# Kernel tuning notes

Hardware: AMD Instinct MI355X
Metric: run time of the kernel (lower is better)

## Reference

```python
import jax, jax.numpy as jnp
import numpy as np

M = 0.25
GAMMA = 256.0
HARD_W = 2.0
O_P = 1.0 + M
O_N = -M
DELTA_P = 1.0 - M
DELTA_N = M
NEG_BIG = -1e30  # masked-out fill for logsumexp (finite to keep grads NaN-free)


def setup_inputs() -> dict:
    key = jax.random.key(0)
    k1, k2 = jax.random.split(key)
    inputs = jax.random.normal(k1, (4096, 512), dtype=jnp.float32)
    targets = jax.random.randint(k2, (4096,), 0, 64, dtype=jnp.int64)
    return {"inputs": inputs, "targets": targets}


def reference(inputs, targets):
    n = inputs.shape[0]
    x = inputs / jnp.linalg.norm(inputs, axis=1, keepdims=True)  # L2 normalize
    sim = x @ x.T                                                # [n, n]

    same = targets[:, None] == targets[None, :]
    eye = jnp.eye(n, dtype=bool)
    pos_mask = same & ~eye
    neg_mask = ~same
    npos = pos_mask.sum(axis=1)
    nneg = neg_mask.sum(axis=1)

    sim_d = jax.lax.stop_gradient(sim)  # alphas are detached in the original
    alpha_p = jax.nn.relu(O_P - sim_d)
    alpha_n = jax.nn.relu(sim_d - O_N)

    # hard mining: scale alpha at hardest positive (min sim) / hardest negative (max sim)
    idx = jnp.arange(n)
    hard_p = jnp.argmin(jnp.where(pos_mask, sim_d, jnp.inf), axis=1)
    hard_n = jnp.argmax(jnp.where(neg_mask, sim_d, -jnp.inf), axis=1)
    hit_p = (idx[None, :] == hard_p[:, None]) & (npos > 1)[:, None]
    hit_n = (idx[None, :] == hard_n[:, None]) & (nneg > 1)[:, None]
    alpha_p = alpha_p * jnp.where(hit_p, HARD_W, 1.0)
    alpha_n = alpha_n * jnp.where(hit_n, HARD_W, 1.0)

    pos_term = jnp.where(pos_mask, -GAMMA * alpha_p * (sim - DELTA_P), NEG_BIG)
    neg_term = jnp.where(neg_mask, GAMMA * alpha_n * (sim - DELTA_N), NEG_BIG)
    lse_p = jax.nn.logsumexp(pos_term, axis=1)
    lse_n = jax.nn.logsumexp(neg_term, axis=1)

    valid = (npos > 0) & (nneg > 0)
    per_row = jnp.where(valid, jax.nn.softplus(lse_p + lse_n), 0.0)
    n_valid = jnp.maximum(valid.sum(), 1)
    return per_row.sum() / n_valid.astype(per_row.dtype)
```

## Files before the change

kernel.cpp:

```cpp
#include <hip/hip_runtime.h>


#define GAMMA_ 256.0f
#define MASKT_  (-1.0e4f)
#define MINITP_ (-1.0e4f)
#define MASKP_  (-3.0e4f)

constexpr int N_ = 4096;
constexpr int D_ = 512;
constexpr int AST_ = 520;
constexpr int CCH_ = 16;

typedef __bf16 bf16x8 __attribute__((ext_vector_type(8)));
typedef float  f32x4  __attribute__((ext_vector_type(4)));
typedef const unsigned int __attribute__((address_space(1)))* gp_t;
typedef unsigned int       __attribute__((address_space(3)))* lp_t;

__device__ __forceinline__ float pos_q(float s) {
    float d = s - 1.0f;
    return fmaf(d * d, 256.0f, -16.0f);
}
__device__ __forceinline__ float neg_q(float s) {
    float q = fmaf(s * s, 256.0f, -16.0f);
    return (s >= -0.25f) ? q : 0.0f;
}
__device__ __forceinline__ void lse_merge(float m2, float S2, float& m, float& S) {
    float mm = fmaxf(m, m2);
    S = S * __expf(m - mm) + S2 * __expf(m2 - mm);
    m = mm;
}
__device__ __forceinline__ unsigned short f2bf(float f) {
    unsigned int u = __float_as_uint(f);
    unsigned int r = u + 0x7FFFu + ((u >> 16) & 1u);
    return (unsigned short)(r >> 16);
}

__global__ __launch_bounds__(256) void k_norm(const float* __restrict__ in,
                                              unsigned short* __restrict__ xb,
                                              float* __restrict__ acc) {
    const int row  = blockIdx.x * 4 + (threadIdx.x >> 6);
    const int lane = threadIdx.x & 63;
    const float4* src = (const float4*)(in + (size_t)row * D_) + lane * 2;
    float4 a = src[0], b = src[1];
    float ss = a.x*a.x + a.y*a.y + a.z*a.z + a.w*a.w
             + b.x*b.x + b.y*b.y + b.z*b.z + b.w*b.w;
    #pragma unroll
    for (int d = 32; d >= 1; d >>= 1) ss += __shfl_xor(ss, d);
    float rn = 1.0f / sqrtf(ss);
    float v[8] = {a.x, a.y, a.z, a.w, b.x, b.y, b.z, b.w};
    union { uint4 u; unsigned short us[8]; } pk;
    #pragma unroll
    for (int k = 0; k < 8; ++k) pk.us[k] = f2bf(v[k] * rn);
    *((uint4*)(xb + (size_t)row * D_) + lane) = pk.u;
    if (blockIdx.x == 0 && threadIdx.x < 4) acc[threadIdx.x] = 0.0f;
}

__global__ __launch_bounds__(256, 4) void k_mainG(const unsigned short* __restrict__ xb,
                                                  const int* __restrict__ tg,
                                                  float* __restrict__ part) {
    constexpr int NST = 16;
    __shared__ __align__(16) unsigned short Bs[2][16][AST_];

    const int tid  = threadIdx.x;
    const int wave = tid >> 6, lane = tid & 63;
    const int n16  = lane & 15, quad = lane >> 4;
    const int rg   = (int)blockIdx.x >> 4;
    const int cc   = (int)blockIdx.x & 15;
    const int rowBase = rg * 64 + wave * 16;
    const int colBase = cc * 256;

    bf16x8 af[16];
    {
        const bf16x8* ap = (const bf16x8*)(xb + (size_t)(rowBase + n16) * D_ + quad * 8);
        #pragma unroll
        for (int kk = 0; kk < 16; ++kk) af[kk] = ap[kk * 4];
    }
    int tr[4];
    #pragma unroll
    for (int r = 0; r < 4; ++r) tr[r] = tg[rowBase + quad * 4 + r];

    float m_p[4], S_p[4], m_n[4], S_n[4], mxn[4];
    #pragma unroll
    for (int r = 0; r < 4; ++r) {
        m_p[r] = MINITP_; S_p[r] = 0.f; m_n[r] = 0.f; S_n[r] = 0.f; mxn[r] = -2.0f;
    }

    const char* gstage = (const char*)xb + (size_t)colBase * 1024 + lane * 16;

    #pragma unroll
    for (int p = 0; p < 4; ++p) {
        int j = p * 4 + wave;
        __builtin_amdgcn_global_load_lds((gp_t)(const void*)(gstage + j * 1024),
                                         (lp_t)(void*)&Bs[0][j][0], 16, 0, 0);
    }
    int tc_cur = tg[colBase + n16];

    auto epi = [&](const f32x4& a0, const f32x4& a1, int tcv, bool withDiag) {
        #pragma unroll
        for (int r = 0; r < 4; ++r) {
            float sim = a0[r] + a1[r];
            bool samec = (tr[r] == tcv);
            float u = samec ? (sim - 1.0f) : sim;
            float t = fmaf(u * u, 256.0f, -16.0f);
            if (!samec && sim < -0.25f) t = 0.0f;
            if (withDiag && n16 == quad * 4 + r) t = MASKP_;
            float ms = samec ? m_p[r] : m_n[r];
            if (t > ms) {
                float scl = __expf(ms - t);
                if (samec) { S_p[r] = fmaf(S_p[r], scl, 1.0f); m_p[r] = t; }
                else       { S_n[r] = fmaf(S_n[r], scl, 1.0f); m_n[r] = t; }
            } else {
                float e = __expf(t - ms);
                S_p[r] += samec ? e : 0.0f;
                S_n[r] += samec ? 0.0f : e;
            }
            mxn[r] = fmaxf(mxn[r], samec ? -2.0f : sim);
        }
    };

    #pragma unroll 1
    for (int s = 0; s < NST; ++s) {
        const int b = s & 1;
        const int j0 = colBase + s * 16;
        __syncthreads();

        if (s + 1 < NST) {
            const char* g2 = gstage + (size_t)(s + 1) * 16 * 1024;
            #pragma unroll
            for (int p = 0; p < 4; ++p) {
                int j = p * 4 + wave;
                __builtin_amdgcn_global_load_lds((gp_t)(const void*)(g2 + j * 1024),
                                                 (lp_t)(void*)&Bs[b ^ 1][j][0], 16, 0, 0);
            }
        }
        int tc_nxt = (s + 1 < NST) ? tg[colBase + (s + 1) * 16 + n16] : 0;

        f32x4 a0 = {0.f, 0.f, 0.f, 0.f}, a1 = {0.f, 0.f, 0.f, 0.f};
        #pragma unroll
        for (int kk = 0; kk < 8; ++kk) {
            bf16x8 bf0 = *(const bf16x8*)&Bs[b][n16][(2 * kk) * 32 + quad * 8];
            bf16x8 bf1 = *(const bf16x8*)&Bs[b][n16][(2 * kk + 1) * 32 + quad * 8];
            a0 = __builtin_amdgcn_mfma_f32_16x16x32_bf16(af[2 * kk],     bf0, a0, 0, 0, 0);
            a1 = __builtin_amdgcn_mfma_f32_16x16x32_bf16(af[2 * kk + 1], bf1, a1, 0, 0, 0);
        }

        if (j0 == rowBase) epi(a0, a1, tc_cur, true);
        else               epi(a0, a1, tc_cur, false);
        tc_cur = tc_nxt;
    }

    #pragma unroll
    for (int r = 0; r < 4; ++r) {
        #pragma unroll
        for (int d = 1; d <= 8; d <<= 1) {
            lse_merge(__shfl_xor(m_p[r], d), __shfl_xor(S_p[r], d), m_p[r], S_p[r]);
            lse_merge(__shfl_xor(m_n[r], d), __shfl_xor(S_n[r], d), m_n[r], S_n[r]);
            mxn[r] = fmaxf(mxn[r], __shfl_xor(mxn[r], d));
        }
    }
    if (n16 == 0) {
        #pragma unroll
        for (int r = 0; r < 4; ++r) {
            ((float4*)part)[(size_t)(rowBase + quad * 4 + r) * CCH_ + cc] =
                make_float4(m_p[r], S_p[r], mxn[r], S_n[r]);
        }
    }
}

__global__ __launch_bounds__(256) void k_reduceF(const float* __restrict__ part,
                                                 const int* __restrict__ tg,
                                                 float* __restrict__ acc,
                                                 float* __restrict__ out) {
    __shared__ int hist[64];
    const int tid = threadIdx.x;
    if (tid < 64) hist[tid] = 0;
    __syncthreads();
    for (int i = tid; i < N_; i += 256) atomicAdd(&hist[tg[i]], 1);
    __syncthreads();

    const int row = blockIdx.x * 256 + tid;
    const float4* P = (const float4*)part + (size_t)row * CCH_;
    float M_p = MINITP_, Sp = 0.f, M_n = 0.f, Sn = 0.f, mxn = -2.0f;
    #pragma unroll
    for (int c = 0; c < CCH_; ++c) {
        float4 a = P[c];
        lse_merge(a.x, a.y, M_p, Sp);
        float mn = (a.z > -1.5f) ? fmaxf(neg_q(a.z), 0.0f) : 0.0f;
        lse_merge(mn, a.w, M_n, Sn);
        mxn = fmaxf(mxn, a.z);
    }
    const int cnt = hist[tg[row]];
    float np2 = (float)(cnt - 1), nn2 = (float)(N_ - cnt);
    float loss = 0.f, vld = 0.f;
    if (np2 > 0.5f && nn2 > 0.5f) {
        if (np2 > 1.5f) {
            float t1 = M_p, t2 = 2.0f * t1;
            float mm = fmaxf(M_p, t2);
            Sp = Sp * __expf(M_p - mm) + __expf(t2 - mm) - __expf(t1 - mm);
            M_p = mm;
        }
        if (nn2 > 1.5f) {
            float t1 = neg_q(mxn), t2 = 2.0f * t1;
            float mm = fmaxf(M_n, t2);
            Sn = Sn * __expf(M_n - mm) + __expf(t2 - mm) - __expf(t1 - mm);
            M_n = mm;
        }
        float z = (M_p + __logf(Sp)) + (M_n + __logf(Sn));
        loss = fmaxf(z, 0.0f) + log1pf(__expf(-fabsf(z)));
        vld = 1.0f;
    }
    #pragma unroll
    for (int d = 32; d >= 1; d >>= 1) { loss += __shfl_xor(loss, d); vld += __shfl_xor(vld, d); }
    if ((tid & 63) == 0) { atomicAdd(&acc[0], loss); atomicAdd(&acc[1], vld); }

    __syncthreads();
    if (tid == 0) {
        __threadfence();
        int old = atomicAdd((int*)(acc + 2), 1);
        if (old == (int)gridDim.x - 1) {
            float ls = atomicAdd(&acc[0], 0.0f);
            float lv = atomicAdd(&acc[1], 0.0f);
            out[0] = ls / fmaxf(lv, 1.0f);
        }
    }
}

__global__ void k_final(const float* __restrict__ acc, float* __restrict__ out) {
    if (threadIdx.x == 0) out[0] = acc[0] / fmaxf(acc[1], 1.0f);
}

__global__ void k_sentinel(float* __restrict__ out) {
    if (threadIdx.x == 0) out[0] = -12345.0f;
}

__global__ __launch_bounds__(1024, 4) void k_main3(const unsigned short* __restrict__ xb,
                                                   const int* __restrict__ tg,
                                                   float* __restrict__ acc_g) {
    __shared__ __align__(16) unsigned short As[16 * AST_];
    __shared__ float sm[16][16][8];
    const int tid  = threadIdx.x;
    const int wave = tid >> 6, lane = tid & 63;
    const int n16  = lane & 15, quad = lane >> 4;
    const int rowBase = blockIdx.x * 16;
    {
        int row = tid >> 6, c = tid & 63;
        *(uint4*)&As[row * AST_ + c * 8] =
            *(const uint4*)(xb + (size_t)(rowBase + row) * D_ + c * 8);
    }
    int ir[4], tr[4];
    #pragma unroll
    for (int r = 0; r < 4; ++r) { ir[r] = rowBase + quad * 4 + r; tr[r] = tg[ir[r]]; }
    float m_p[4], S_p[4], m_n[4], S_n[4], mnp[4], mxn[4], sc[4];
    #pragma unroll
    for (int r = 0; r < 4; ++r) {
        m_p[r] = 0.f; S_p[r] = 0.f; m_n[r] = 0.f; S_n[r] = 0.f;
        mnp[r] = 2.0f; mxn[r] = -2.0f; sc[r] = 0.f;
    }
    __syncthreads();
    const unsigned short* Af = &As[n16 * AST_ + quad * 8];
    #pragma unroll 1
    for (int t = wave; t < N_ / 16; t += 16) {
        const int jcol = t * 16 + n16;
        const int tc = tg[jcol];
        const bf16x8* bp = (const bf16x8*)(xb + (size_t)jcol * D_ + quad * 8);
        bf16x8 bf[16];
        #pragma unroll
        for (int kk = 0; kk < 16; ++kk) bf[kk] = bp[kk * 4];
        f32x4 a0 = {0.f, 0.f, 0.f, 0.f}, a1 = {0.f, 0.f, 0.f, 0.f};
        #pragma unroll
        for (int kk = 0; kk < 8; ++kk) {
            bf16x8 af0 = *(const bf16x8*)(Af + (2 * kk) * 32);
            bf16x8 af1 = *(const bf16x8*)(Af + (2 * kk + 1) * 32);
            a0 = __builtin_amdgcn_mfma_f32_16x16x32_bf16(af0, bf[2 * kk],     a0, 0, 0, 0);
            a1 = __builtin_amdgcn_mfma_f32_16x16x32_bf16(af1, bf[2 * kk + 1], a1, 0, 0, 0);
        }
        #pragma unroll
        for (int r = 0; r < 4; ++r) {
            float s = a0[r] + a1[r];
            bool samec = (tr[r] == tc);
            bool posm  = samec && (jcol != ir[r]);
            float tp = posm  ? pos_q(s) : MASKT_;
            float tn = samec ? MASKT_ : neg_q(s);
            float mm = fmaxf(m_p[r], tp);
            S_p[r] = S_p[r] * __expf(m_p[r] - mm) + __expf(tp - mm); m_p[r] = mm;
            mm = fmaxf(m_n[r], tn);
            S_n[r] = S_n[r] * __expf(m_n[r] - mm) + __expf(tn - mm); m_n[r] = mm;
            sc[r] += samec ? 1.0f : 0.0f;
            mnp[r] = fminf(mnp[r], posm ? s : 2.0f);
            mxn[r] = fmaxf(mxn[r], samec ? -2.0f : s);
        }
    }
    #pragma unroll
    for (int r = 0; r < 4; ++r) {
        #pragma unroll
        for (int d = 1; d <= 8; d <<= 1) {
            lse_merge(__shfl_xor(m_p[r], d), __shfl_xor(S_p[r], d), m_p[r], S_p[r]);
            lse_merge(__shfl_xor(m_n[r], d), __shfl_xor(S_n[r], d), m_n[r], S_n[r]);
            mnp[r] = fminf(mnp[r], __shfl_xor(mnp[r], d));
            mxn[r] = fmaxf(mxn[r], __shfl_xor(mxn[r], d));
            sc[r] += __shfl_xor(sc[r], d);
        }
    }
    if (n16 == 0) {
        #pragma unroll
        for (int r = 0; r < 4; ++r) {
            float* q = sm[wave][quad * 4 + r];
            q[0] = m_p[r]; q[1] = S_p[r]; q[2] = m_n[r]; q[3] = S_n[r];
            q[4] = mnp[r]; q[5] = mxn[r]; q[6] = sc[r];
        }
    }
    __syncthreads();
    if (tid < 64) {
        const int L = tid & 15;
        float m_p2 = 0.f, S_p2 = 0.f, m_n2 = 0.f, S_n2 = 0.f;
        float mnp2 = 2.0f, mxn2 = -2.0f, sct = 0.f;
        #pragma unroll
        for (int w = 0; w < 16; ++w) {
            const float* q = sm[w][L];
            lse_merge(q[0], q[1], m_p2, S_p2);
            lse_merge(q[2], q[3], m_n2, S_n2);
            mnp2 = fminf(mnp2, q[4]); mxn2 = fmaxf(mxn2, q[5]);
            sct += q[6];
        }
        float loss = 0.f, vld = 0.f;
        float np2 = sct - 1.0f, nn2 = (float)N_ - sct;
        if (tid < 16 && np2 > 0.5f && nn2 > 0.5f) {
            if (np2 > 1.5f) {
                float t1 = pos_q(mnp2), t2 = 2.0f * t1;
                float mm = fmaxf(m_p2, t2);
                S_p2 = S_p2 * __expf(m_p2 - mm) + __expf(t2 - mm) - __expf(t1 - mm);
                m_p2 = mm;
            }
            if (nn2 > 1.5f) {
                float t1 = neg_q(mxn2), t2 = 2.0f * t1;
                float mm = fmaxf(m_n2, t2);
                S_n2 = S_n2 * __expf(m_n2 - mm) + __expf(t2 - mm) - __expf(t1 - mm);
                m_n2 = mm;
            }
            float z = (m_p2 + __logf(S_p2)) + (m_n2 + __logf(S_n2));
            loss = fmaxf(z, 0.0f) + log1pf(__expf(-fabsf(z)));
            vld = 1.0f;
        }
        #pragma unroll
        for (int d = 32; d >= 1; d >>= 1) {
            loss += __shfl_xor(loss, d); vld += __shfl_xor(vld, d);
        }
        if (tid == 0) { atomicAdd(&acc_g[0], loss); atomicAdd(&acc_g[1], vld); }
    }
}

extern "C" void kernel_launch(void* const* d_in, const int* in_sizes, int n_in,
                              void* d_out, int out_size, void* d_ws, size_t ws_size,
                              hipStream_t stream) {
    const float* in = (const float*)d_in[0];
    const int*   tg = (const int*)d_in[1];
    constexpr size_t MB = 1024 * 1024;
    unsigned short* xb = (unsigned short*)d_ws;

    if (ws_size >= 5 * MB + 64) {
        float* part = (float*)((char*)d_ws + 4 * MB);
        float* acc  = (float*)((char*)d_ws + 5 * MB);
        hipLaunchKernelGGL(k_norm,    dim3(N_ / 4),    dim3(256), 0, stream, in, xb, acc);
        hipLaunchKernelGGL(k_mainG,   dim3(64 * CCH_), dim3(256), 0, stream, xb, tg, part);
        hipLaunchKernelGGL(k_reduceF, dim3(N_ / 256),  dim3(256), 0, stream, part, tg, acc,
                           (float*)d_out);
    } else if (ws_size >= 4 * MB + 64) {
        float* acc = (float*)((char*)d_ws + 4 * MB);
        hipLaunchKernelGGL(k_norm,  dim3(N_ / 4),  dim3(256),  0, stream, in, xb, acc);
        hipLaunchKernelGGL(k_main3, dim3(N_ / 16), dim3(1024), 0, stream, xb, tg, acc);
        hipLaunchKernelGGL(k_final, dim3(1),       dim3(64),   0, stream, acc, (float*)d_out);
    } else {
        hipLaunchKernelGGL(k_sentinel, dim3(1), dim3(64), 0, stream, (float*)d_out);
    }
}
```

Before: 106.9 us.

## Compute 32 rows per wave to reuse each LDS B tile twice

Each wave now holds two 16-row A fragment sets and runs four MFMA chains per 16-column step against the same LDS B tile. This halves the grid size and the number of times each column tile is staged and read per row. The cost is doubled A-fragment and accumulator register state, with launch bounds lowered to 2 blocks per CU. That reduces occupancy and the latency hiding available for the exp-heavy epilogue.

```diff
diff --git a/kernel.cpp b/kernel.cpp
--- a/kernel.cpp
+++ b/kernel.cpp
@@ -55,7 +55,7 @@
     if (blockIdx.x == 0 && threadIdx.x < 4) acc[threadIdx.x] = 0.0f;
 }
 
-__global__ __launch_bounds__(256, 4) void k_mainG(const unsigned short* __restrict__ xb,
+__global__ __launch_bounds__(256, 2) void k_mainH(const unsigned short* __restrict__ xb,
                                                   const int* __restrict__ tg,
                                                   float* __restrict__ part) {
     constexpr int NST = 16;
@@ -66,23 +66,26 @@
     const int n16  = lane & 15, quad = lane >> 4;
     const int rg   = (int)blockIdx.x >> 4;
     const int cc   = (int)blockIdx.x & 15;
-    const int rowBase = rg * 64 + wave * 16;
+    const int rowBase = rg * 128 + wave * 32;
     const int colBase = cc * 256;
 
-    bf16x8 af[16];
+    bf16x8 af0[16], af1[16];
     {
-        const bf16x8* ap = (const bf16x8*)(xb + (size_t)(rowBase + n16) * D_ + quad * 8);
-        #pragma unroll
-        for (int kk = 0; kk < 16; ++kk) af[kk] = ap[kk * 4];
-    }
-    int tr[4];
-    #pragma unroll
-    for (int r = 0; r < 4; ++r) tr[r] = tg[rowBase + quad * 4 + r];
-
-    float m_p[4], S_p[4], m_n[4], S_n[4], mxn[4];
-    #pragma unroll
-    for (int r = 0; r < 4; ++r) {
-        m_p[r] = MINITP_; S_p[r] = 0.f; m_n[r] = 0.f; S_n[r] = 0.f; mxn[r] = -2.0f;
+        const bf16x8* ap0 = (const bf16x8*)(xb + (size_t)(rowBase + n16) * D_ + quad * 8);
+        const bf16x8* ap1 = (const bf16x8*)(xb + (size_t)(rowBase + 16 + n16) * D_ + quad * 8);
+        #pragma unroll
+        for (int kk = 0; kk < 16; ++kk) { af0[kk] = ap0[kk * 4]; af1[kk] = ap1[kk * 4]; }
+    }
+    int tr[8];
+    #pragma unroll
+    for (int g = 0; g < 2; ++g)
+        #pragma unroll
+        for (int r = 0; r < 4; ++r) tr[g * 4 + r] = tg[rowBase + g * 16 + quad * 4 + r];
+
+    float m_p[8], S_p[8], m_n[8], S_n[8], mxn[8];
+    #pragma unroll
+    for (int i = 0; i < 8; ++i) {
+        m_p[i] = MINITP_; S_p[i] = 0.f; m_n[i] = 0.f; S_n[i] = 0.f; mxn[i] = -2.0f;
     }
 
     const char* gstage = (const char*)xb + (size_t)colBase * 1024 + lane * 16;
@@ -95,26 +98,26 @@
     }
     int tc_cur = tg[colBase + n16];
 
-    auto epi = [&](const f32x4& a0, const f32x4& a1, int tcv, bool withDiag) {
+    auto epi = [&](const f32x4& a0, const f32x4& a1, int tcv, bool withDiag, int base) {
         #pragma unroll
         for (int r = 0; r < 4; ++r) {
             float sim = a0[r] + a1[r];
-            bool samec = (tr[r] == tcv);
+            bool samec = (tr[base + r] == tcv);
             float u = samec ? (sim - 1.0f) : sim;
             float t = fmaf(u * u, 256.0f, -16.0f);
             if (!samec && sim < -0.25f) t = 0.0f;
             if (withDiag && n16 == quad * 4 + r) t = MASKP_;
-            float ms = samec ? m_p[r] : m_n[r];
+            float ms = samec ? m_p[base + r] : m_n[base + r];
             if (t > ms) {
                 float scl = __expf(ms - t);
-                if (samec) { S_p[r] = fmaf(S_p[r], scl, 1.0f); m_p[r] = t; }
-                else       { S_n[r] = fmaf(S_n[r], scl, 1.0f); m_n[r] = t; }
+                if (samec) { S_p[base + r] = fmaf(S_p[base + r], scl, 1.0f); m_p[base + r] = t; }
+                else       { S_n[base + r] = fmaf(S_n[base + r], scl, 1.0f); m_n[base + r] = t; }
             } else {
                 float e = __expf(t - ms);
-                S_p[r] += samec ? e : 0.0f;
-                S_n[r] += samec ? 0.0f : e;
-            }
-            mxn[r] = fmaxf(mxn[r], samec ? -2.0f : sim);
+                S_p[base + r] += samec ? e : 0.0f;
+                S_n[base + r] += samec ? 0.0f : e;
+            }
+            mxn[base + r] = fmaxf(mxn[base + r], samec ? -2.0f : sim);
         }
     };
 
@@ -136,34 +139,42 @@
         int tc_nxt = (s + 1 < NST) ? tg[colBase + (s + 1) * 16 + n16] : 0;
 
         f32x4 a0 = {0.f, 0.f, 0.f, 0.f}, a1 = {0.f, 0.f, 0.f, 0.f};
+        f32x4 a2 = {0.f, 0.f, 0.f, 0.f}, a3 = {0.f, 0.f, 0.f, 0.f};
         #pragma unroll
         for (int kk = 0; kk < 8; ++kk) {
             bf16x8 bf0 = *(const bf16x8*)&Bs[b][n16][(2 * kk) * 32 + quad * 8];
             bf16x8 bf1 = *(const bf16x8*)&Bs[b][n16][(2 * kk + 1) * 32 + quad * 8];
-            a0 = __builtin_amdgcn_mfma_f32_16x16x32_bf16(af[2 * kk],     bf0, a0, 0, 0, 0);
-            a1 = __builtin_amdgcn_mfma_f32_16x16x32_bf16(af[2 * kk + 1], bf1, a1, 0, 0, 0);
-        }
-
-        if (j0 == rowBase) epi(a0, a1, tc_cur, true);
-        else               epi(a0, a1, tc_cur, false);
+            a0 = __builtin_amdgcn_mfma_f32_16x16x32_bf16(af0[2 * kk],     bf0, a0, 0, 0, 0);
+            a1 = __builtin_amdgcn_mfma_f32_16x16x32_bf16(af0[2 * kk + 1], bf1, a1, 0, 0, 0);
+            a2 = __builtin_amdgcn_mfma_f32_16x16x32_bf16(af1[2 * kk],     bf0, a2, 0, 0, 0);
+            a3 = __builtin_amdgcn_mfma_f32_16x16x32_bf16(af1[2 * kk + 1], bf1, a3, 0, 0, 0);
+        }
+
+        if (j0 == rowBase)      epi(a0, a1, tc_cur, true,  0);
+        else                    epi(a0, a1, tc_cur, false, 0);
+        if (j0 == rowBase + 16) epi(a2, a3, tc_cur, true,  4);
+        else                    epi(a2, a3, tc_cur, false, 4);
         tc_cur = tc_nxt;
     }
 
     #pragma unroll
-    for (int r = 0; r < 4; ++r) {
+    for (int i = 0; i < 8; ++i) {
         #pragma unroll
         for (int d = 1; d <= 8; d <<= 1) {
-            lse_merge(__shfl_xor(m_p[r], d), __shfl_xor(S_p[r], d), m_p[r], S_p[r]);
-            lse_merge(__shfl_xor(m_n[r], d), __shfl_xor(S_n[r], d), m_n[r], S_n[r]);
-            mxn[r] = fmaxf(mxn[r], __shfl_xor(mxn[r], d));
+            lse_merge(__shfl_xor(m_p[i], d), __shfl_xor(S_p[i], d), m_p[i], S_p[i]);
+            lse_merge(__shfl_xor(m_n[i], d), __shfl_xor(S_n[i], d), m_n[i], S_n[i]);
+            mxn[i] = fmaxf(mxn[i], __shfl_xor(mxn[i], d));
         }
     }
     if (n16 == 0) {
         #pragma unroll
-        for (int r = 0; r < 4; ++r) {
-            ((float4*)part)[(size_t)(rowBase + quad * 4 + r) * CCH_ + cc] =
-                make_float4(m_p[r], S_p[r], mxn[r], S_n[r]);
-        }
+        for (int g = 0; g < 2; ++g)
+            #pragma unroll
+            for (int r = 0; r < 4; ++r) {
+                int i = g * 4 + r;
+                ((float4*)part)[(size_t)(rowBase + g * 16 + quad * 4 + r) * CCH_ + cc] =
+                    make_float4(m_p[i], S_p[i], mxn[i], S_n[i]);
+            }
     }
 }
 
@@ -361,7 +372,7 @@
         float* part = (float*)((char*)d_ws + 4 * MB);
         float* acc  = (float*)((char*)d_ws + 5 * MB);
         hipLaunchKernelGGL(k_norm,    dim3(N_ / 4),    dim3(256), 0, stream, in, xb, acc);
-        hipLaunchKernelGGL(k_mainG,   dim3(64 * CCH_), dim3(256), 0, stream, xb, tg, part);
+        hipLaunchKernelGGL(k_mainH,   dim3(32 * CCH_), dim3(256), 0, stream, xb, tg, part);
         hipLaunchKernelGGL(k_reduceF, dim3(N_ / 256),  dim3(256), 0, stream, part, tg, acc,
                            (float*)d_out);
     } else if (ws_size >= 4 * MB + 64) {
```

After: 110.2 us. 1.03x slower.

## Use base-2 exponent domain, stagger column tile order, raise MFMA priority

Applied to the files above, without the earlier changes.

Rescales the quadratic logit constants by 1/ln2 so every exponential becomes a native exp2 instead of __expf, which saves a multiply per exp in the hot epilogue. The log-sum-exp state now lives in the base-2 domain throughout, and the final value is converted back to natural log. It also rotates each block's starting column tile by a phase taken from the block index, spreading concurrent blocks across different B tiles to reduce L2/channel contention. It also sets s_setprio around the MFMA loop. These add complexity, and the constant rescaling carries a small rounding risk.

```diff
diff --git a/kernel.cpp b/kernel.cpp
--- a/kernel.cpp
+++ b/kernel.cpp
@@ -1,10 +1,12 @@
 #include <hip/hip_runtime.h>
 
 
-#define GAMMA_ 256.0f
 #define MASKT_  (-1.0e4f)
 #define MINITP_ (-1.0e4f)
 #define MASKP_  (-3.0e4f)
+#define QA_     369.3299304675f
+#define QB_     (-23.08312065422f)
+#define LN2_    0.6931471805599453f
 
 constexpr int N_ = 4096;
 constexpr int D_ = 512;
@@ -24,9 +26,18 @@
     float q = fmaf(s * s, 256.0f, -16.0f);
     return (s >= -0.25f) ? q : 0.0f;
 }
+__device__ __forceinline__ float neg_q2(float s) {
+    float q = fmaf(s * s, QA_, QB_);
+    return (s >= -0.25f) ? q : 0.0f;
+}
 __device__ __forceinline__ void lse_merge(float m2, float S2, float& m, float& S) {
     float mm = fmaxf(m, m2);
     S = S * __expf(m - mm) + S2 * __expf(m2 - mm);
+    m = mm;
+}
+__device__ __forceinline__ void lse_merge2(float m2, float S2, float& m, float& S) {
+    float mm = fmaxf(m, m2);
+    S = S * exp2f(m - mm) + S2 * exp2f(m2 - mm);
     m = mm;
 }
 __device__ __forceinline__ unsigned short f2bf(float f) {
@@ -55,7 +66,7 @@
     if (blockIdx.x == 0 && threadIdx.x < 4) acc[threadIdx.x] = 0.0f;
 }
 
-__global__ __launch_bounds__(256, 4) void k_mainG(const unsigned short* __restrict__ xb,
+__global__ __launch_bounds__(256, 4) void k_mainJ(const unsigned short* __restrict__ xb,
                                                   const int* __restrict__ tg,
                                                   float* __restrict__ part) {
     constexpr int NST = 16;
@@ -68,6 +79,7 @@
     const int cc   = (int)blockIdx.x & 15;
     const int rowBase = rg * 64 + wave * 16;
     const int colBase = cc * 256;
+    const int phase = (((int)blockIdx.x >> 8) & 3) * 4;
 
     bf16x8 af[16];
     {
@@ -87,13 +99,16 @@
 
     const char* gstage = (const char*)xb + (size_t)colBase * 1024 + lane * 16;
 
-    #pragma unroll
-    for (int p = 0; p < 4; ++p) {
-        int j = p * 4 + wave;
-        __builtin_amdgcn_global_load_lds((gp_t)(const void*)(gstage + j * 1024),
-                                         (lp_t)(void*)&Bs[0][j][0], 16, 0, 0);
-    }
-    int tc_cur = tg[colBase + n16];
+    {
+        const char* g0 = gstage + (size_t)phase * 16384;
+        #pragma unroll
+        for (int p = 0; p < 4; ++p) {
+            int j = p * 4 + wave;
+            __builtin_amdgcn_global_load_lds((gp_t)(const void*)(g0 + j * 1024),
+                                             (lp_t)(void*)&Bs[0][j][0], 16, 0, 0);
+        }
+    }
+    int tc_cur = tg[colBase + phase * 16 + n16];
 
     auto epi = [&](const f32x4& a0, const f32x4& a1, int tcv, bool withDiag) {
         #pragma unroll
@@ -101,16 +116,16 @@
             float sim = a0[r] + a1[r];
             bool samec = (tr[r] == tcv);
             float u = samec ? (sim - 1.0f) : sim;
-            float t = fmaf(u * u, 256.0f, -16.0f);
+            float t = fmaf(u * u, QA_, QB_);
             if (!samec && sim < -0.25f) t = 0.0f;
             if (withDiag && n16 == quad * 4 + r) t = MASKP_;
             float ms = samec ? m_p[r] : m_n[r];
             if (t > ms) {
-                float scl = __expf(ms - t);
+                float scl = exp2f(ms - t);
                 if (samec) { S_p[r] = fmaf(S_p[r], scl, 1.0f); m_p[r] = t; }
                 else       { S_n[r] = fmaf(S_n[r], scl, 1.0f); m_n[r] = t; }
             } else {
-                float e = __expf(t - ms);
+                float e = exp2f(t - ms);
                 S_p[r] += samec ? e : 0.0f;
                 S_n[r] += samec ? 0.0f : e;
             }
@@ -119,13 +134,15 @@
     };
 
     #pragma unroll 1
-    for (int s = 0; s < NST; ++s) {
-        const int b = s & 1;
+    for (int u = 0; u < NST; ++u) {
+        const int s = (u + phase) & 15;
+        const int b = u & 1;
         const int j0 = colBase + s * 16;
         __syncthreads();
 
-        if (s + 1 < NST) {
-            const char* g2 = gstage + (size_t)(s + 1) * 16 * 1024;
+        const int sn = (s + 1) & 15;
+        if (u + 1 < NST) {
+            const char* g2 = gstage + (size_t)sn * 16384;
             #pragma unroll
             for (int p = 0; p < 4; ++p) {
                 int j = p * 4 + wave;
@@ -133,9 +150,10 @@
                                                  (lp_t)(void*)&Bs[b ^ 1][j][0], 16, 0, 0);
             }
         }
-        int tc_nxt = (s + 1 < NST) ? tg[colBase + (s + 1) * 16 + n16] : 0;
+        int tc_nxt = (u + 1 < NST) ? tg[colBase + sn * 16 + n16] : 0;
 
         f32x4 a0 = {0.f, 0.f, 0.f, 0.f}, a1 = {0.f, 0.f, 0.f, 0.f};
+        __builtin_amdgcn_s_setprio(1);
         #pragma unroll
         for (int kk = 0; kk < 8; ++kk) {
             bf16x8 bf0 = *(const bf16x8*)&Bs[b][n16][(2 * kk) * 32 + quad * 8];
@@ -143,6 +161,7 @@
             a0 = __builtin_amdgcn_mfma_f32_16x16x32_bf16(af[2 * kk],     bf0, a0, 0, 0, 0);
             a1 = __builtin_amdgcn_mfma_f32_16x16x32_bf16(af[2 * kk + 1], bf1, a1, 0, 0, 0);
         }
+        __builtin_amdgcn_s_setprio(0);
 
         if (j0 == rowBase) epi(a0, a1, tc_cur, true);
         else               epi(a0, a1, tc_cur, false);
@@ -153,8 +172,8 @@
     for (int r = 0; r < 4; ++r) {
         #pragma unroll
         for (int d = 1; d <= 8; d <<= 1) {
-            lse_merge(__shfl_xor(m_p[r], d), __shfl_xor(S_p[r], d), m_p[r], S_p[r]);
-            lse_merge(__shfl_xor(m_n[r], d), __shfl_xor(S_n[r], d), m_n[r], S_n[r]);
+            lse_merge2(__shfl_xor(m_p[r], d), __shfl_xor(S_p[r], d), m_p[r], S_p[r]);
+            lse_merge2(__shfl_xor(m_n[r], d), __shfl_xor(S_n[r], d), m_n[r], S_n[r]);
             mxn[r] = fmaxf(mxn[r], __shfl_xor(mxn[r], d));
         }
     }
@@ -184,9 +203,9 @@
     #pragma unroll
     for (int c = 0; c < CCH_; ++c) {
         float4 a = P[c];
-        lse_merge(a.x, a.y, M_p, Sp);
-        float mn = (a.z > -1.5f) ? fmaxf(neg_q(a.z), 0.0f) : 0.0f;
-        lse_merge(mn, a.w, M_n, Sn);
+        lse_merge2(a.x, a.y, M_p, Sp);
+        float mn = (a.z > -1.5f) ? fmaxf(neg_q2(a.z), 0.0f) : 0.0f;
+        lse_merge2(mn, a.w, M_n, Sn);
         mxn = fmaxf(mxn, a.z);
     }
     const int cnt = hist[tg[row]];
@@ -196,16 +215,16 @@
         if (np2 > 1.5f) {
             float t1 = M_p, t2 = 2.0f * t1;
             float mm = fmaxf(M_p, t2);
-            Sp = Sp * __expf(M_p - mm) + __expf(t2 - mm) - __expf(t1 - mm);
+            Sp = Sp * exp2f(M_p - mm) + exp2f(t2 - mm) - exp2f(t1 - mm);
             M_p = mm;
         }
         if (nn2 > 1.5f) {
-            float t1 = neg_q(mxn), t2 = 2.0f * t1;
+            float t1 = neg_q2(mxn), t2 = 2.0f * t1;
             float mm = fmaxf(M_n, t2);
-            Sn = Sn * __expf(M_n - mm) + __expf(t2 - mm) - __expf(t1 - mm);
+            Sn = Sn * exp2f(M_n - mm) + exp2f(t2 - mm) - exp2f(t1 - mm);
             M_n = mm;
         }
-        float z = (M_p + __logf(Sp)) + (M_n + __logf(Sn));
+        float z = LN2_ * ((M_p + __log2f(Sp)) + (M_n + __log2f(Sn)));
         loss = fmaxf(z, 0.0f) + log1pf(__expf(-fabsf(z)));
         vld = 1.0f;
     }
@@ -361,7 +380,7 @@
         float* part = (float*)((char*)d_ws + 4 * MB);
         float* acc  = (float*)((char*)d_ws + 5 * MB);
         hipLaunchKernelGGL(k_norm,    dim3(N_ / 4),    dim3(256), 0, stream, in, xb, acc);
-        hipLaunchKernelGGL(k_mainG,   dim3(64 * CCH_), dim3(256), 0, stream, xb, tg, part);
+        hipLaunchKernelGGL(k_mainJ,   dim3(64 * CCH_), dim3(256), 0, stream, xb, tg, part);
         hipLaunchKernelGGL(k_reduceF, dim3(N_ / 256),  dim3(256), 0, stream, part, tg, acc,
                            (float*)d_out);
     } else if (ws_size >= 4 * MB + 64) {
```

New measurement: 109.2 us. +2.1%, slower.
